# Kernel optimization log

Measured on AMD Instinct MI355X. Metric: run time of the kernel, lower is better.

The kernel has to match this reference:

```python
import jax, jax.numpy as jnp
import numpy as np

H = 4            # num_heads (forced: 128 projection / d_k=32)
DK = 32          # hardcoded d_k
SCALE = 1.0 / np.sqrt(32.0)
EPS = 1e-5       # LayerNorm eps (torch default)


def setup_inputs() -> dict:
    key = jax.random.key(0)
    ks = jax.random.split(key, 8)
    B, L, Dq, Dkv, M = 16, 4096, 512, 512, 512
    def w(k, shape, fan_in):
        return (jax.random.normal(k, shape, jnp.float32) / np.sqrt(fan_in)).astype(jnp.float32)
    return {
        "Q_in":  jax.random.normal(ks[0], (B, L, Dq),  jnp.float32),
        "KV_in": jax.random.normal(ks[1], (B, L, Dkv), jnp.float32),
        "Wq":  w(ks[2], (Dq, 128), Dq),   "bq":  jnp.zeros((128,), jnp.float32),
        "Wk":  w(ks[3], (Dkv, 128), Dkv), "bk":  jnp.zeros((128,), jnp.float32),
        "Wv":  w(ks[4], (Dkv, 128), Dkv), "bv":  jnp.zeros((128,), jnp.float32),
        "Wo":  w(ks[5], (128, M), 128),   "bo":  jnp.zeros((M,), jnp.float32),
        "Wqo": w(ks[6], (128, M), 128),   "bqo": jnp.zeros((M,), jnp.float32),
        "gamma": jnp.ones((M,), jnp.float32),
        "beta":  jnp.zeros((M,), jnp.float32),
    }


def reference(Q_in, KV_in, Wq, bq, Wk, bk, Wv, bv, Wo, bo, Wqo, bqo, gamma, beta):
    B, L, _ = Q_in.shape
    Qm = Q_in @ Wq + bq          # (B, L, 128)
    Km = KV_in @ Wk + bk         # (B, L, 128)
    Vm = KV_in @ Wv + bv         # (B, L, 128)

    def heads(X):
        # view(B, L, H, DK).permute(0, 2, 3, 1) -> (B, H, DK, L)
        return X.reshape(B, L, H, DK).transpose(0, 2, 3, 1)

    Qh, Kh, Vh = heads(Qm), heads(Km), heads(Vm)
    # matmul contracts over the SEQUENCE dim -> feature-feature scores (B,H,DK,DK)
    scores = jnp.einsum('bhdl,bhel->bhde', Qh, Kh) * SCALE
    attn = jax.nn.softmax(scores, axis=-1)          # dropout = identity (eval)
    out_h = jnp.einsum('bhde,bhel->bhdl', attn, Vh)  # (B, H, DK, L)
    out_h = out_h.transpose(0, 3, 1, 2).reshape(B, L, H * DK)  # (B, L, 128)

    out = out_h @ Wo + bo        # (B, L, M)
    Qm_ = Qm @ Wqo + bqo         # (B, L, M)
    x = Qm_ + out
    mu = jnp.mean(x, axis=-1, keepdims=True)
    var = jnp.var(x, axis=-1, keepdims=True)
    y = (x - mu) * jax.lax.rsqrt(var + EPS) * gamma + beta
    return (y, attn)
```

## Files before the change

### kernel.cpp

```cpp
#include <hip/hip_runtime.h>
#include <hip/hip_bf16.h>

typedef __bf16 bf16x8 __attribute__((ext_vector_type(8)));
typedef float  f32x4  __attribute__((ext_vector_type(4)));

#define SCALE_QK 0.17677669529663687f
#define LDSS 40

__device__ __forceinline__ float b2f(ushort u) {
    __hip_bfloat16 h; *reinterpret_cast<ushort*>(&h) = u; return __bfloat162float(h);
}
__device__ __forceinline__ ushort f2b(float f) {
    __hip_bfloat16 h = __float2bfloat16(f); return *reinterpret_cast<ushort*>(&h);
}

__global__ void k_prep(const float* __restrict__ Wq, const float* __restrict__ Wk,
                       const float* __restrict__ Wv, const float* __restrict__ Wqo,
                       const float* __restrict__ Wo,
                       ushort* __restrict__ WqThi, ushort* __restrict__ WqTlo,
                       ushort* __restrict__ WkThi, ushort* __restrict__ WkTlo,
                       ushort* __restrict__ WvT,  ushort* __restrict__ WqoT,
                       ushort* __restrict__ WoB) {
    int idx = blockIdx.x * 256 + threadIdx.x;
    int mat = idx >> 16, i = idx & 65535;
    if (mat == 0) {
        int n = i >> 9, k = i & 511;
        float w = Wq[k * 128 + n];
        ushort hi = f2b(w);
        WqThi[i] = hi; WqTlo[i] = f2b(w - b2f(hi));
    } else if (mat == 1) {
        int n = i >> 9, k = i & 511;
        float w = Wk[k * 128 + n];
        ushort hi = f2b(w);
        WkThi[i] = hi; WkTlo[i] = f2b(w - b2f(hi));
    } else if (mat == 2) {
        int n = i >> 9, k = i & 511;
        WvT[i] = f2b(Wv[k * 128 + n]);
    } else if (mat == 3) {
        int n = i >> 7, k = i & 127;
        WqoT[i] = f2b(Wqo[k * 512 + n]);
    } else if (mat == 4) {
        WoB[i] = f2b(Wo[i]);
    }
}

__global__ __launch_bounds__(256) void k_proj_split(
        const float* __restrict__ A, const ushort* __restrict__ BThi,
        const ushort* __restrict__ BTlo, const float* __restrict__ bias,
        float* __restrict__ outF, ushort* __restrict__ outB) {
    __shared__ __align__(16) ushort AsH[128 * LDSS], AsL[128 * LDSS];
    __shared__ __align__(16) ushort BsH[128 * LDSS], BsL[128 * LDSS];
    const int row0 = blockIdx.x * 128;
    const int tid  = threadIdx.x;
    const int wid  = tid >> 6, lane = tid & 63;
    const int wm = wid >> 1, wn = wid & 1;
    const int quad = lane >> 4, l16 = lane & 15;
    const int sr = tid >> 2;
    const int sc = (tid & 3) * 8;

    f32x4 acc[4][4] = {};

    for (int k0 = 0; k0 < 512; k0 += 32) {
        __syncthreads();
#pragma unroll
        for (int p = 0; p < 2; ++p) {
            int r = sr + p * 64;
            float4 a0 = *(const float4*)&A[(size_t)(row0 + r) * 512 + k0 + sc];
            float4 a1 = *(const float4*)&A[(size_t)(row0 + r) * 512 + k0 + sc + 4];
            float av[8] = {a0.x, a0.y, a0.z, a0.w, a1.x, a1.y, a1.z, a1.w};
            union { uint4 v; ushort u[8]; } H, L;
#pragma unroll
            for (int i = 0; i < 8; ++i) {
                ushort hi = f2b(av[i]);
                H.u[i] = hi;
                L.u[i] = f2b(av[i] - b2f(hi));
            }
            *(uint4*)&AsH[r * LDSS + sc] = H.v;
            *(uint4*)&AsL[r * LDSS + sc] = L.v;
            *(uint4*)&BsH[r * LDSS + sc] = *(const uint4*)&BThi[(size_t)r * 512 + k0 + sc];
            *(uint4*)&BsL[r * LDSS + sc] = *(const uint4*)&BTlo[(size_t)r * 512 + k0 + sc];
        }
        __syncthreads();
        bf16x8 aH[4], aL[4];
#pragma unroll
        for (int i = 0; i < 4; ++i) {
            int ro = (wm * 64 + i * 16 + l16) * LDSS + quad * 8;
            aH[i] = *reinterpret_cast<const bf16x8*>(&AsH[ro]);
            aL[i] = *reinterpret_cast<const bf16x8*>(&AsL[ro]);
        }
#pragma unroll
        for (int j = 0; j < 4; ++j) {
            int ro = (wn * 64 + j * 16 + l16) * LDSS + quad * 8;
            bf16x8 bH = *reinterpret_cast<const bf16x8*>(&BsH[ro]);
            bf16x8 bL = *reinterpret_cast<const bf16x8*>(&BsL[ro]);
#pragma unroll
            for (int i = 0; i < 4; ++i) {
                acc[i][j] = __builtin_amdgcn_mfma_f32_16x16x32_bf16(aL[i], bH, acc[i][j], 0, 0, 0);
                acc[i][j] = __builtin_amdgcn_mfma_f32_16x16x32_bf16(aH[i], bL, acc[i][j], 0, 0, 0);
                acc[i][j] = __builtin_amdgcn_mfma_f32_16x16x32_bf16(aH[i], bH, acc[i][j], 0, 0, 0);
            }
        }
    }

#pragma unroll
    for (int i = 0; i < 4; ++i)
#pragma unroll
        for (int j = 0; j < 4; ++j) {
            int ncol = wn * 64 + j * 16 + l16;
            float bv = bias[ncol];
#pragma unroll
            for (int r = 0; r < 4; ++r) {
                int mrow = row0 + wm * 64 + i * 16 + quad * 4 + r;
                float v = acc[i][j][r] + bv;
                if (outF) outF[(size_t)mrow * 128 + ncol] = v;
                if (outB) outB[(size_t)mrow * 128 + ncol] = f2b(v);
            }
        }
}

__global__ __launch_bounds__(256) void k_proj_kv(
        const float* __restrict__ A,
        const ushort* __restrict__ BKhi, const ushort* __restrict__ BKlo,
        const ushort* __restrict__ BV,
        const float* __restrict__ biasK, const float* __restrict__ biasV,
        float* __restrict__ KmF, ushort* __restrict__ VmB) {
    __shared__ __align__(16) ushort AsH[128 * LDSS], AsL[128 * LDSS];
    __shared__ __align__(16) ushort BsKH[128 * LDSS], BsKL[128 * LDSS], BsV[128 * LDSS];
    const int row0 = blockIdx.x * 128;
    const int tid  = threadIdx.x;
    const int wid  = tid >> 6, lane = tid & 63;
    const int wm = wid >> 1, wn = wid & 1;
    const int quad = lane >> 4, l16 = lane & 15;
    const int sr = tid >> 2;
    const int sc = (tid & 3) * 8;

    f32x4 accK[4][4] = {};
    f32x4 accV[4][4] = {};

    for (int k0 = 0; k0 < 512; k0 += 32) {
        __syncthreads();
#pragma unroll
        for (int p = 0; p < 2; ++p) {
            int r = sr + p * 64;
            float4 a0 = *(const float4*)&A[(size_t)(row0 + r) * 512 + k0 + sc];
            float4 a1 = *(const float4*)&A[(size_t)(row0 + r) * 512 + k0 + sc + 4];
            float av[8] = {a0.x, a0.y, a0.z, a0.w, a1.x, a1.y, a1.z, a1.w};
            union { uint4 v; ushort u[8]; } H, L;
#pragma unroll
            for (int i = 0; i < 8; ++i) {
                ushort hi = f2b(av[i]);
                H.u[i] = hi;
                L.u[i] = f2b(av[i] - b2f(hi));
            }
            *(uint4*)&AsH[r * LDSS + sc] = H.v;
            *(uint4*)&AsL[r * LDSS + sc] = L.v;
            *(uint4*)&BsKH[r * LDSS + sc] = *(const uint4*)&BKhi[(size_t)r * 512 + k0 + sc];
            *(uint4*)&BsKL[r * LDSS + sc] = *(const uint4*)&BKlo[(size_t)r * 512 + k0 + sc];
            *(uint4*)&BsV [r * LDSS + sc] = *(const uint4*)&BV  [(size_t)r * 512 + k0 + sc];
        }
        __syncthreads();
        bf16x8 aH[4], aL[4];
#pragma unroll
        for (int i = 0; i < 4; ++i) {
            int ro = (wm * 64 + i * 16 + l16) * LDSS + quad * 8;
            aH[i] = *reinterpret_cast<const bf16x8*>(&AsH[ro]);
            aL[i] = *reinterpret_cast<const bf16x8*>(&AsL[ro]);
        }
#pragma unroll
        for (int j = 0; j < 4; ++j) {
            int ro = (wn * 64 + j * 16 + l16) * LDSS + quad * 8;
            bf16x8 bKH = *reinterpret_cast<const bf16x8*>(&BsKH[ro]);
            bf16x8 bKL = *reinterpret_cast<const bf16x8*>(&BsKL[ro]);
            bf16x8 bV  = *reinterpret_cast<const bf16x8*>(&BsV [ro]);
#pragma unroll
            for (int i = 0; i < 4; ++i) {
                accK[i][j] = __builtin_amdgcn_mfma_f32_16x16x32_bf16(aL[i], bKH, accK[i][j], 0, 0, 0);
                accK[i][j] = __builtin_amdgcn_mfma_f32_16x16x32_bf16(aH[i], bKL, accK[i][j], 0, 0, 0);
                accK[i][j] = __builtin_amdgcn_mfma_f32_16x16x32_bf16(aH[i], bKH, accK[i][j], 0, 0, 0);
                accV[i][j] = __builtin_amdgcn_mfma_f32_16x16x32_bf16(aH[i], bV,  accV[i][j], 0, 0, 0);
            }
        }
    }

#pragma unroll
    for (int i = 0; i < 4; ++i)
#pragma unroll
        for (int j = 0; j < 4; ++j) {
            int ncol = wn * 64 + j * 16 + l16;
            float bk = biasK[ncol], bv = biasV[ncol];
#pragma unroll
            for (int r = 0; r < 4; ++r) {
                int mrow = row0 + wm * 64 + i * 16 + quad * 4 + r;
                KmF[(size_t)mrow * 128 + ncol] = accK[i][j][r] + bk;
                VmB[(size_t)mrow * 128 + ncol] = f2b(accV[i][j][r] + bv);
            }
        }
}

__global__ __launch_bounds__(256) void k_scores(
        const float* __restrict__ Qm, const float* __restrict__ Km,
        float* __restrict__ partial) {
    int b = blockIdx.x, sp = blockIdx.y;
    int t = threadIdx.x;
    int h = t >> 6, tl = t & 63;
    int d0 = (tl >> 3) * 4, e0 = (tl & 7) * 4;
    const float* Qb = Qm + ((size_t)b * 4096 + sp * 128) * 128 + h * 32 + d0;
    const float* Kb = Km + ((size_t)b * 4096 + sp * 128) * 128 + h * 32 + e0;
    float acc[4][4] = {};
#pragma unroll 4
    for (int l = 0; l < 128; ++l) {
        float4 q4 = *(const float4*)(Qb + (size_t)l * 128);
        float4 k4 = *(const float4*)(Kb + (size_t)l * 128);
        float q[4] = {q4.x, q4.y, q4.z, q4.w};
        float k[4] = {k4.x, k4.y, k4.z, k4.w};
#pragma unroll
        for (int i = 0; i < 4; ++i)
#pragma unroll
            for (int j = 0; j < 4; ++j) acc[i][j] += q[i] * k[j];
    }
    float* P = partial + ((size_t)(sp * 64 + b * 4 + h)) * 1024;
#pragma unroll
    for (int i = 0; i < 4; ++i)
#pragma unroll
        for (int j = 0; j < 4; ++j)
            P[(d0 + i) * 32 + e0 + j] = acc[i][j];
}

__global__ __launch_bounds__(256) void k_attn(
        const float* __restrict__ partial, const ushort* __restrict__ WoB,
        float* __restrict__ attnOut, ushort* __restrict__ WcT) {
    int bh = blockIdx.x; int b = bh >> 2, h = bh & 3;
    __shared__ float aS[1024];
    __shared__ __align__(16) ushort wS[32 * 512];
    int t = threadIdx.x;
    for (int i = t; i < 1024; i += 256) {
        float s = 0.f;
#pragma unroll
        for (int sp = 0; sp < 32; ++sp)
            s += partial[(size_t)(sp * 64 + bh) * 1024 + i];
        aS[i] = s * SCALE_QK;
    }
    for (int i = t; i < 2048; i += 256) {
        int r = i >> 6, c = (i & 63) * 8;
        *(uint4*)&wS[r * 512 + c] = *(const uint4*)&WoB[(size_t)(h * 32 + r) * 512 + c];
    }
    __syncthreads();
    if (t < 32) {
        float m = -1e30f;
#pragma unroll
        for (int e = 0; e < 32; ++e) m = fmaxf(m, aS[t * 32 + e]);
        float p[32]; float sum = 0.f;
#pragma unroll
        for (int e = 0; e < 32; ++e) { p[e] = __expf(aS[t * 32 + e] - m); sum += p[e]; }
        float inv = 1.f / sum;
#pragma unroll
        for (int e = 0; e < 32; ++e) aS[t * 32 + e] = p[e] * inv;
    }
    __syncthreads();
    for (int i = t; i < 1024; i += 256)
        attnOut[(size_t)bh * 1024 + i] = aS[i];
    int e = t & 31, mg = t >> 5;
    for (int mi = 0; mi < 64; ++mi) {
        int m = mg * 64 + mi;
        float acc = 0.f;
#pragma unroll
        for (int d = 0; d < 32; ++d)
            acc += aS[d * 32 + e] * b2f(wS[d * 512 + m]);
        WcT[((size_t)b * 512 + m) * 128 + h * 32 + e] = f2b(acc);
    }
}

__global__ __launch_bounds__(256) void k_out_ln(
        const ushort* __restrict__ Vm, const ushort* __restrict__ Qm,
        const ushort* __restrict__ WcT, const ushort* __restrict__ WqoT,
        const float* __restrict__ bo, const float* __restrict__ bqo,
        const float* __restrict__ gamma, const float* __restrict__ beta,
        float* __restrict__ Y) {
    __shared__ __align__(16) ushort As[64 * LDSS];
    __shared__ __align__(16) ushort Bs[512 * LDSS];
    __shared__ float sumS[4][64], sumSS[4][64], muA[64], rsA[64];
    const int row0 = blockIdx.x * 64;
    const int b = row0 >> 12;
    const ushort* WcTb = WcT + (size_t)b * 512 * 128;
    const int tid = threadIdx.x;
    const int wid = tid >> 6, lane = tid & 63;
    const int quad = lane >> 4, l16 = lane & 15;
    const int sr = tid >> 2;
    const int sc = (tid & 3) * 8;

    f32x4 acc[4][8] = {};

    for (int k0 = 0; k0 < 256; k0 += 32) {
        const ushort* Asrc; const ushort* Bsrc; int kk;
        if (k0 < 128) { Asrc = Vm; Bsrc = WcTb; kk = k0; }
        else          { Asrc = Qm; Bsrc = WqoT; kk = k0 - 128; }
        __syncthreads();
        *(uint4*)&As[sr * LDSS + sc] =
            *(const uint4*)&Asrc[(size_t)(row0 + sr) * 128 + kk + sc];
#pragma unroll
        for (int p = 0; p < 8; ++p) {
            int r = sr + p * 64;
            *(uint4*)&Bs[r * LDSS + sc] = *(const uint4*)&Bsrc[(size_t)r * 128 + kk + sc];
        }
        __syncthreads();
        bf16x8 aF[4];
#pragma unroll
        for (int i = 0; i < 4; ++i)
            aF[i] = *reinterpret_cast<const bf16x8*>(&As[(i * 16 + l16) * LDSS + quad * 8]);
#pragma unroll
        for (int j = 0; j < 8; ++j) {
            bf16x8 bF = *reinterpret_cast<const bf16x8*>(
                &Bs[(wid * 128 + j * 16 + l16) * LDSS + quad * 8]);
#pragma unroll
            for (int i = 0; i < 4; ++i)
                acc[i][j] = __builtin_amdgcn_mfma_f32_16x16x32_bf16(aF[i], bF, acc[i][j], 0, 0, 0);
        }
    }

    float bv[8];
#pragma unroll
    for (int j = 0; j < 8; ++j) {
        int ncol = wid * 128 + j * 16 + l16;
        bv[j] = bo[ncol] + bqo[ncol];
    }
    float sArr[4][4], ssArr[4][4];
#pragma unroll
    for (int i = 0; i < 4; ++i)
#pragma unroll
        for (int r = 0; r < 4; ++r) {
            float s = 0.f, ss = 0.f;
#pragma unroll
            for (int j = 0; j < 8; ++j) {
                float x = acc[i][j][r] + bv[j];
                s += x; ss += x * x;
            }
            sArr[i][r] = s; ssArr[i][r] = ss;
        }
#pragma unroll
    for (int off = 1; off < 16; off <<= 1)
#pragma unroll
        for (int i = 0; i < 4; ++i)
#pragma unroll
            for (int r = 0; r < 4; ++r) {
                sArr[i][r]  += __shfl_xor(sArr[i][r],  off, 64);
                ssArr[i][r] += __shfl_xor(ssArr[i][r], off, 64);
            }
    if (l16 == 0) {
#pragma unroll
        for (int i = 0; i < 4; ++i)
#pragma unroll
            for (int r = 0; r < 4; ++r) {
                int row = i * 16 + quad * 4 + r;
                sumS[wid][row]  = sArr[i][r];
                sumSS[wid][row] = ssArr[i][r];
            }
    }
    __syncthreads();
    if (tid < 64) {
        float s = sumS[0][tid] + sumS[1][tid] + sumS[2][tid] + sumS[3][tid];
        float ss = sumSS[0][tid] + sumSS[1][tid] + sumSS[2][tid] + sumSS[3][tid];
        float mu = s * (1.f / 512.f);
        float var = ss * (1.f / 512.f) - mu * mu;
        muA[tid] = mu;
        rsA[tid] = rsqrtf(var + 1e-5f);
    }
    __syncthreads();

    float gj[8], bj[8];
#pragma unroll
    for (int j = 0; j < 8; ++j) {
        int ncol = wid * 128 + j * 16 + l16;
        gj[j] = gamma[ncol]; bj[j] = beta[ncol];
    }
#pragma unroll
    for (int i = 0; i < 4; ++i)
#pragma unroll
        for (int r = 0; r < 4; ++r) {
            int row = i * 16 + quad * 4 + r;
            float mu = muA[row], rstd = rsA[row];
            size_t base = (size_t)(row0 + row) * 512 + wid * 128 + l16;
#pragma unroll
            for (int j = 0; j < 8; ++j) {
                float x = acc[i][j][r] + bv[j];
                Y[base + j * 16] = (x - mu) * rstd * gj[j] + bj[j];
            }
        }
}

extern "C" void kernel_launch(void* const* d_in, const int* in_sizes, int n_in,
                              void* d_out, int out_size, void* d_ws, size_t ws_size,
                              hipStream_t stream) {
    const float* Qin   = (const float*)d_in[0];
    const float* KVin  = (const float*)d_in[1];
    const float* Wq    = (const float*)d_in[2];
    const float* bq    = (const float*)d_in[3];
    const float* Wk    = (const float*)d_in[4];
    const float* bk    = (const float*)d_in[5];
    const float* Wv    = (const float*)d_in[6];
    const float* bv    = (const float*)d_in[7];
    const float* Wo    = (const float*)d_in[8];
    const float* bo    = (const float*)d_in[9];
    const float* Wqo   = (const float*)d_in[10];
    const float* bqo   = (const float*)d_in[11];
    const float* gamma = (const float*)d_in[12];
    const float* beta  = (const float*)d_in[13];
    float* out = (float*)d_out;
    float* attnOut = out + 33554432;

    char* ws = (char*)d_ws;
    ushort* WqThi = (ushort*)(ws);
    ushort* WqTlo = (ushort*)(ws + 131072);
    ushort* WkThi = (ushort*)(ws + 262144);
    ushort* WkTlo = (ushort*)(ws + 393216);
    ushort* WvT   = (ushort*)(ws + 524288);
    ushort* WqoT  = (ushort*)(ws + 655360);
    ushort* WoB   = (ushort*)(ws + 786432);
    float*  QmF   = (float*) (ws + 917504);
    float*  KmF   = (float*) (ws + 34471936);
    ushort* QmB   = (ushort*)(ws + 68026368);
    ushort* VmB   = (ushort*)(ws + 84803584);
    float*  part  = (float*) (ws + 101580800);
    ushort* WcT   = (ushort*)(ws + 109969408);

    k_prep<<<1280, 256, 0, stream>>>(Wq, Wk, Wv, Wqo, Wo,
                                     WqThi, WqTlo, WkThi, WkTlo, WvT, WqoT, WoB);
    k_proj_split<<<512, 256, 0, stream>>>(Qin, WqThi, WqTlo, bq, QmF, QmB);
    k_proj_kv<<<512, 256, 0, stream>>>(KVin, WkThi, WkTlo, WvT, bk, bv, KmF, VmB);
    k_scores<<<dim3(16, 32), 256, 0, stream>>>(QmF, KmF, part);
    k_attn<<<64, 256, 0, stream>>>(part, WoB, attnOut, WcT);
    k_out_ln<<<1024, 256, 0, stream>>>(VmB, QmB, WcT, WqoT, bo, bqo, gamma, beta, out);
}
```

Before: 485.9 us.

## Drop LDS staging in projection and output GEMMs; load fragments directly per wave

The projection and output/LayerNorm kernels no longer stage tiles in shared memory with block barriers. Each wave now owns 16 rows, loads its A fragment straight from global memory, and streams B (weight) fragments directly from global/L2. The LayerNorm reduction becomes wave-local, with no cross-wave shared-memory reduction. The scores kernel's sequence split is doubled (64 chunks of 64) for more blocks, and the workspace offset is moved to fit the larger partial buffer. This removes barriers and LDS traffic but gives up weight reuse across waves, so weight reads rise, and k_out_ln's 32 accumulators increase register pressure.

```diff
diff --git a/kernel.cpp b/kernel.cpp
--- a/kernel.cpp
+++ b/kernel.cpp
@@ -5,13 +5,27 @@
 typedef float  f32x4  __attribute__((ext_vector_type(4)));
 
 #define SCALE_QK 0.17677669529663687f
-#define LDSS 40
+#define MFMA(a, b, c) __builtin_amdgcn_mfma_f32_16x16x32_bf16((a), (b), (c), 0, 0, 0)
 
 __device__ __forceinline__ float b2f(ushort u) {
     __hip_bfloat16 h; *reinterpret_cast<ushort*>(&h) = u; return __bfloat162float(h);
 }
 __device__ __forceinline__ ushort f2b(float f) {
     __hip_bfloat16 h = __float2bfloat16(f); return *reinterpret_cast<ushort*>(&h);
+}
+__device__ __forceinline__ bf16x8 ld8(const ushort* p) {
+    union { uint4 v; bf16x8 f; } u; u.v = *(const uint4*)p; return u.f;
+}
+__device__ __forceinline__ void split8(float4 a0, float4 a1, bf16x8& hi, bf16x8& lo) {
+    float av[8] = {a0.x, a0.y, a0.z, a0.w, a1.x, a1.y, a1.z, a1.w};
+    union { bf16x8 f; ushort u[8]; } H, L;
+#pragma unroll
+    for (int i = 0; i < 8; ++i) {
+        ushort h = f2b(av[i]);
+        H.u[i] = h;
+        L.u[i] = f2b(av[i] - b2f(h));
+    }
+    hi = H.f; lo = L.f;
 }
 
 __global__ void k_prep(const float* __restrict__ Wq, const float* __restrict__ Wk,
@@ -44,78 +58,47 @@
     }
 }
 
-__global__ __launch_bounds__(256) void k_proj_split(
+__global__ __launch_bounds__(256) void k_proj_q(
         const float* __restrict__ A, const ushort* __restrict__ BThi,
         const ushort* __restrict__ BTlo, const float* __restrict__ bias,
         float* __restrict__ outF, ushort* __restrict__ outB) {
-    __shared__ __align__(16) ushort AsH[128 * LDSS], AsL[128 * LDSS];
-    __shared__ __align__(16) ushort BsH[128 * LDSS], BsL[128 * LDSS];
-    const int row0 = blockIdx.x * 128;
-    const int tid  = threadIdx.x;
-    const int wid  = tid >> 6, lane = tid & 63;
-    const int wm = wid >> 1, wn = wid & 1;
+    const int tid = threadIdx.x;
+    const int w = tid >> 6, lane = tid & 63;
     const int quad = lane >> 4, l16 = lane & 15;
-    const int sr = tid >> 2;
-    const int sc = (tid & 3) * 8;
-
-    f32x4 acc[4][4] = {};
+    const int wrow0 = blockIdx.x * 64 + w * 16;
+    const float* Ar = A + (size_t)(wrow0 + l16) * 512 + quad * 8;
+
+    f32x4 acc[8] = {};
 
     for (int k0 = 0; k0 < 512; k0 += 32) {
-        __syncthreads();
-#pragma unroll
-        for (int p = 0; p < 2; ++p) {
-            int r = sr + p * 64;
-            float4 a0 = *(const float4*)&A[(size_t)(row0 + r) * 512 + k0 + sc];
-            float4 a1 = *(const float4*)&A[(size_t)(row0 + r) * 512 + k0 + sc + 4];
-            float av[8] = {a0.x, a0.y, a0.z, a0.w, a1.x, a1.y, a1.z, a1.w};
-            union { uint4 v; ushort u[8]; } H, L;
-#pragma unroll
-            for (int i = 0; i < 8; ++i) {
-                ushort hi = f2b(av[i]);
-                H.u[i] = hi;
-                L.u[i] = f2b(av[i] - b2f(hi));
-            }
-            *(uint4*)&AsH[r * LDSS + sc] = H.v;
-            *(uint4*)&AsL[r * LDSS + sc] = L.v;
-            *(uint4*)&BsH[r * LDSS + sc] = *(const uint4*)&BThi[(size_t)r * 512 + k0 + sc];
-            *(uint4*)&BsL[r * LDSS + sc] = *(const uint4*)&BTlo[(size_t)r * 512 + k0 + sc];
-        }
-        __syncthreads();
-        bf16x8 aH[4], aL[4];
-#pragma unroll
-        for (int i = 0; i < 4; ++i) {
-            int ro = (wm * 64 + i * 16 + l16) * LDSS + quad * 8;
-            aH[i] = *reinterpret_cast<const bf16x8*>(&AsH[ro]);
-            aL[i] = *reinterpret_cast<const bf16x8*>(&AsL[ro]);
-        }
-#pragma unroll
-        for (int j = 0; j < 4; ++j) {
-            int ro = (wn * 64 + j * 16 + l16) * LDSS + quad * 8;
-            bf16x8 bH = *reinterpret_cast<const bf16x8*>(&BsH[ro]);
-            bf16x8 bL = *reinterpret_cast<const bf16x8*>(&BsL[ro]);
-#pragma unroll
-            for (int i = 0; i < 4; ++i) {
-                acc[i][j] = __builtin_amdgcn_mfma_f32_16x16x32_bf16(aL[i], bH, acc[i][j], 0, 0, 0);
-                acc[i][j] = __builtin_amdgcn_mfma_f32_16x16x32_bf16(aH[i], bL, acc[i][j], 0, 0, 0);
-                acc[i][j] = __builtin_amdgcn_mfma_f32_16x16x32_bf16(aH[i], bH, acc[i][j], 0, 0, 0);
-            }
-        }
-    }
-
-#pragma unroll
-    for (int i = 0; i < 4; ++i)
-#pragma unroll
-        for (int j = 0; j < 4; ++j) {
-            int ncol = wn * 64 + j * 16 + l16;
-            float bv = bias[ncol];
-#pragma unroll
-            for (int r = 0; r < 4; ++r) {
-                int mrow = row0 + wm * 64 + i * 16 + quad * 4 + r;
-                float v = acc[i][j][r] + bv;
-                if (outF) outF[(size_t)mrow * 128 + ncol] = v;
-                if (outB) outB[(size_t)mrow * 128 + ncol] = f2b(v);
-            }
-        }
+        float4 a0 = *(const float4*)(Ar + k0);
+        float4 a1 = *(const float4*)(Ar + k0 + 4);
+        bf16x8 aH, aL;
+        split8(a0, a1, aH, aL);
+        const int bofs = k0 + quad * 8;
+#pragma unroll
+        for (int j = 0; j < 8; ++j) {
+            const size_t bro = (size_t)(j * 16 + l16) * 512 + bofs;
+            bf16x8 bH = ld8(&BThi[bro]);
+            bf16x8 bL = ld8(&BTlo[bro]);
+            acc[j] = MFMA(aL, bH, acc[j]);
+            acc[j] = MFMA(aH, bL, acc[j]);
+            acc[j] = MFMA(aH, bH, acc[j]);
+        }
+    }
+
+    const int rbase = wrow0 + quad * 4;
+#pragma unroll
+    for (int j = 0; j < 8; ++j) {
+        int col = j * 16 + l16;
+        float bv = bias[col];
+#pragma unroll
+        for (int r = 0; r < 4; ++r) {
+            float v = acc[j][r] + bv;
+            outF[(size_t)(rbase + r) * 128 + col] = v;
+            outB[(size_t)(rbase + r) * 128 + col] = f2b(v);
+        }
+    }
 }
 
 __global__ __launch_bounds__(256) void k_proj_kv(
@@ -124,77 +107,45 @@
         const ushort* __restrict__ BV,
         const float* __restrict__ biasK, const float* __restrict__ biasV,
         float* __restrict__ KmF, ushort* __restrict__ VmB) {
-    __shared__ __align__(16) ushort AsH[128 * LDSS], AsL[128 * LDSS];
-    __shared__ __align__(16) ushort BsKH[128 * LDSS], BsKL[128 * LDSS], BsV[128 * LDSS];
-    const int row0 = blockIdx.x * 128;
-    const int tid  = threadIdx.x;
-    const int wid  = tid >> 6, lane = tid & 63;
-    const int wm = wid >> 1, wn = wid & 1;
+    const int tid = threadIdx.x;
+    const int w = tid >> 6, lane = tid & 63;
     const int quad = lane >> 4, l16 = lane & 15;
-    const int sr = tid >> 2;
-    const int sc = (tid & 3) * 8;
-
-    f32x4 accK[4][4] = {};
-    f32x4 accV[4][4] = {};
+    const int wrow0 = blockIdx.x * 64 + w * 16;
+    const float* Ar = A + (size_t)(wrow0 + l16) * 512 + quad * 8;
+
+    f32x4 accK[8] = {};
+    f32x4 accV[8] = {};
 
     for (int k0 = 0; k0 < 512; k0 += 32) {
-        __syncthreads();
-#pragma unroll
-        for (int p = 0; p < 2; ++p) {
-            int r = sr + p * 64;
-            float4 a0 = *(const float4*)&A[(size_t)(row0 + r) * 512 + k0 + sc];
-            float4 a1 = *(const float4*)&A[(size_t)(row0 + r) * 512 + k0 + sc + 4];
-            float av[8] = {a0.x, a0.y, a0.z, a0.w, a1.x, a1.y, a1.z, a1.w};
-            union { uint4 v; ushort u[8]; } H, L;
-#pragma unroll
-            for (int i = 0; i < 8; ++i) {
-                ushort hi = f2b(av[i]);
-                H.u[i] = hi;
-                L.u[i] = f2b(av[i] - b2f(hi));
-            }
-            *(uint4*)&AsH[r * LDSS + sc] = H.v;
-            *(uint4*)&AsL[r * LDSS + sc] = L.v;
-            *(uint4*)&BsKH[r * LDSS + sc] = *(const uint4*)&BKhi[(size_t)r * 512 + k0 + sc];
-            *(uint4*)&BsKL[r * LDSS + sc] = *(const uint4*)&BKlo[(size_t)r * 512 + k0 + sc];
-            *(uint4*)&BsV [r * LDSS + sc] = *(const uint4*)&BV  [(size_t)r * 512 + k0 + sc];
-        }
-        __syncthreads();
-        bf16x8 aH[4], aL[4];
-#pragma unroll
-        for (int i = 0; i < 4; ++i) {
-            int ro = (wm * 64 + i * 16 + l16) * LDSS + quad * 8;
-            aH[i] = *reinterpret_cast<const bf16x8*>(&AsH[ro]);
-            aL[i] = *reinterpret_cast<const bf16x8*>(&AsL[ro]);
-        }
-#pragma unroll
-        for (int j = 0; j < 4; ++j) {
-            int ro = (wn * 64 + j * 16 + l16) * LDSS + quad * 8;
-            bf16x8 bKH = *reinterpret_cast<const bf16x8*>(&BsKH[ro]);
-            bf16x8 bKL = *reinterpret_cast<const bf16x8*>(&BsKL[ro]);
-            bf16x8 bV  = *reinterpret_cast<const bf16x8*>(&BsV [ro]);
-#pragma unroll
-            for (int i = 0; i < 4; ++i) {
-                accK[i][j] = __builtin_amdgcn_mfma_f32_16x16x32_bf16(aL[i], bKH, accK[i][j], 0, 0, 0);
-                accK[i][j] = __builtin_amdgcn_mfma_f32_16x16x32_bf16(aH[i], bKL, accK[i][j], 0, 0, 0);
-                accK[i][j] = __builtin_amdgcn_mfma_f32_16x16x32_bf16(aH[i], bKH, accK[i][j], 0, 0, 0);
-                accV[i][j] = __builtin_amdgcn_mfma_f32_16x16x32_bf16(aH[i], bV,  accV[i][j], 0, 0, 0);
-            }
-        }
-    }
-
-#pragma unroll
-    for (int i = 0; i < 4; ++i)
-#pragma unroll
-        for (int j = 0; j < 4; ++j) {
-            int ncol = wn * 64 + j * 16 + l16;
-            float bk = biasK[ncol], bv = biasV[ncol];
-#pragma unroll
-            for (int r = 0; r < 4; ++r) {
-                int mrow = row0 + wm * 64 + i * 16 + quad * 4 + r;
-                KmF[(size_t)mrow * 128 + ncol] = accK[i][j][r] + bk;
-                VmB[(size_t)mrow * 128 + ncol] = f2b(accV[i][j][r] + bv);
-            }
-        }
+        float4 a0 = *(const float4*)(Ar + k0);
+        float4 a1 = *(const float4*)(Ar + k0 + 4);
+        bf16x8 aH, aL;
+        split8(a0, a1, aH, aL);
+        const int bofs = k0 + quad * 8;
+#pragma unroll
+        for (int j = 0; j < 8; ++j) {
+            const size_t bro = (size_t)(j * 16 + l16) * 512 + bofs;
+            bf16x8 bH = ld8(&BKhi[bro]);
+            bf16x8 bL = ld8(&BKlo[bro]);
+            bf16x8 bV = ld8(&BV[bro]);
+            accK[j] = MFMA(aL, bH, accK[j]);
+            accK[j] = MFMA(aH, bL, accK[j]);
+            accK[j] = MFMA(aH, bH, accK[j]);
+            accV[j] = MFMA(aH, bV, accV[j]);
+        }
+    }
+
+    const int rbase = wrow0 + quad * 4;
+#pragma unroll
+    for (int j = 0; j < 8; ++j) {
+        int col = j * 16 + l16;
+        float bk = biasK[col], bv = biasV[col];
+#pragma unroll
+        for (int r = 0; r < 4; ++r) {
+            KmF[(size_t)(rbase + r) * 128 + col] = accK[j][r] + bk;
+            VmB[(size_t)(rbase + r) * 128 + col] = f2b(accV[j][r] + bv);
+        }
+    }
 }
 
 __global__ __launch_bounds__(256) void k_scores(
@@ -204,11 +155,11 @@
     int t = threadIdx.x;
     int h = t >> 6, tl = t & 63;
     int d0 = (tl >> 3) * 4, e0 = (tl & 7) * 4;
-    const float* Qb = Qm + ((size_t)b * 4096 + sp * 128) * 128 + h * 32 + d0;
-    const float* Kb = Km + ((size_t)b * 4096 + sp * 128) * 128 + h * 32 + e0;
+    const float* Qb = Qm + ((size_t)b * 4096 + sp * 64) * 128 + h * 32 + d0;
+    const float* Kb = Km + ((size_t)b * 4096 + sp * 64) * 128 + h * 32 + e0;
     float acc[4][4] = {};
-#pragma unroll 4
-    for (int l = 0; l < 128; ++l) {
+#pragma unroll 8
+    for (int l = 0; l < 64; ++l) {
         float4 q4 = *(const float4*)(Qb + (size_t)l * 128);
         float4 k4 = *(const float4*)(Kb + (size_t)l * 128);
         float q[4] = {q4.x, q4.y, q4.z, q4.w};
@@ -236,7 +187,7 @@
     for (int i = t; i < 1024; i += 256) {
         float s = 0.f;
 #pragma unroll
-        for (int sp = 0; sp < 32; ++sp)
+        for (int sp = 0; sp < 64; ++sp)
             s += partial[(size_t)(sp * 64 + bh) * 1024 + i];
         aS[i] = s * SCALE_QK;
     }
@@ -276,115 +227,64 @@
         const float* __restrict__ bo, const float* __restrict__ bqo,
         const float* __restrict__ gamma, const float* __restrict__ beta,
         float* __restrict__ Y) {
-    __shared__ __align__(16) ushort As[64 * LDSS];
-    __shared__ __align__(16) ushort Bs[512 * LDSS];
-    __shared__ float sumS[4][64], sumSS[4][64], muA[64], rsA[64];
-    const int row0 = blockIdx.x * 64;
-    const int b = row0 >> 12;
+    const int tid = threadIdx.x;
+    const int w = tid >> 6, lane = tid & 63;
+    const int quad = lane >> 4, l16 = lane & 15;
+    const int wrow0 = blockIdx.x * 64 + w * 16;
+    const int b = wrow0 >> 12;
     const ushort* WcTb = WcT + (size_t)b * 512 * 128;
-    const int tid = threadIdx.x;
-    const int wid = tid >> 6, lane = tid & 63;
-    const int quad = lane >> 4, l16 = lane & 15;
-    const int sr = tid >> 2;
-    const int sc = (tid & 3) * 8;
-
-    f32x4 acc[4][8] = {};
-
+
+    f32x4 acc[32] = {};
+
+#pragma unroll
     for (int k0 = 0; k0 < 256; k0 += 32) {
-        const ushort* Asrc; const ushort* Bsrc; int kk;
-        if (k0 < 128) { Asrc = Vm; Bsrc = WcTb; kk = k0; }
-        else          { Asrc = Qm; Bsrc = WqoT; kk = k0 - 128; }
-        __syncthreads();
-        *(uint4*)&As[sr * LDSS + sc] =
-            *(const uint4*)&Asrc[(size_t)(row0 + sr) * 128 + kk + sc];
-#pragma unroll
-        for (int p = 0; p < 8; ++p) {
-            int r = sr + p * 64;
-            *(uint4*)&Bs[r * LDSS + sc] = *(const uint4*)&Bsrc[(size_t)r * 128 + kk + sc];
-        }
-        __syncthreads();
-        bf16x8 aF[4];
-#pragma unroll
-        for (int i = 0; i < 4; ++i)
-            aF[i] = *reinterpret_cast<const bf16x8*>(&As[(i * 16 + l16) * LDSS + quad * 8]);
-#pragma unroll
-        for (int j = 0; j < 8; ++j) {
-            bf16x8 bF = *reinterpret_cast<const bf16x8*>(
-                &Bs[(wid * 128 + j * 16 + l16) * LDSS + quad * 8]);
-#pragma unroll
-            for (int i = 0; i < 4; ++i)
-                acc[i][j] = __builtin_amdgcn_mfma_f32_16x16x32_bf16(aF[i], bF, acc[i][j], 0, 0, 0);
-        }
-    }
-
-    float bv[8];
-#pragma unroll
-    for (int j = 0; j < 8; ++j) {
-        int ncol = wid * 128 + j * 16 + l16;
-        bv[j] = bo[ncol] + bqo[ncol];
-    }
-    float sArr[4][4], ssArr[4][4];
-#pragma unroll
-    for (int i = 0; i < 4; ++i)
+        const ushort* Asrc = (k0 < 128) ? Vm : Qm;
+        const ushort* Bsrc = (k0 < 128) ? WcTb : WqoT;
+        const int kk = (k0 < 128) ? k0 : (k0 - 128);
+        bf16x8 aF = ld8(&Asrc[(size_t)(wrow0 + l16) * 128 + kk + quad * 8]);
+        const int bofs = kk + quad * 8;
+#pragma unroll
+        for (int j = 0; j < 32; ++j) {
+            bf16x8 bF = ld8(&Bsrc[(size_t)(j * 16 + l16) * 128 + bofs]);
+            acc[j] = MFMA(aF, bF, acc[j]);
+        }
+    }
+
+    float s[4] = {0.f, 0.f, 0.f, 0.f}, ss[4] = {0.f, 0.f, 0.f, 0.f};
+#pragma unroll
+    for (int j = 0; j < 32; ++j) {
+        int col = j * 16 + l16;
+        float bv = bo[col] + bqo[col];
 #pragma unroll
         for (int r = 0; r < 4; ++r) {
-            float s = 0.f, ss = 0.f;
-#pragma unroll
-            for (int j = 0; j < 8; ++j) {
-                float x = acc[i][j][r] + bv[j];
-                s += x; ss += x * x;
-            }
-            sArr[i][r] = s; ssArr[i][r] = ss;
-        }
+            float x = acc[j][r] + bv;
+            acc[j][r] = x;
+            s[r] += x; ss[r] += x * x;
+        }
+    }
 #pragma unroll
     for (int off = 1; off < 16; off <<= 1)
 #pragma unroll
-        for (int i = 0; i < 4; ++i)
-#pragma unroll
-            for (int r = 0; r < 4; ++r) {
-                sArr[i][r]  += __shfl_xor(sArr[i][r],  off, 64);
-                ssArr[i][r] += __shfl_xor(ssArr[i][r], off, 64);
-            }
-    if (l16 == 0) {
-#pragma unroll
-        for (int i = 0; i < 4; ++i)
-#pragma unroll
-            for (int r = 0; r < 4; ++r) {
-                int row = i * 16 + quad * 4 + r;
-                sumS[wid][row]  = sArr[i][r];
-                sumSS[wid][row] = ssArr[i][r];
-            }
-    }
-    __syncthreads();
-    if (tid < 64) {
-        float s = sumS[0][tid] + sumS[1][tid] + sumS[2][tid] + sumS[3][tid];
-        float ss = sumSS[0][tid] + sumSS[1][tid] + sumSS[2][tid] + sumSS[3][tid];
-        float mu = s * (1.f / 512.f);
-        float var = ss * (1.f / 512.f) - mu * mu;
-        muA[tid] = mu;
-        rsA[tid] = rsqrtf(var + 1e-5f);
-    }
-    __syncthreads();
-
-    float gj[8], bj[8];
-#pragma unroll
-    for (int j = 0; j < 8; ++j) {
-        int ncol = wid * 128 + j * 16 + l16;
-        gj[j] = gamma[ncol]; bj[j] = beta[ncol];
-    }
-#pragma unroll
-    for (int i = 0; i < 4; ++i)
-#pragma unroll
         for (int r = 0; r < 4; ++r) {
-            int row = i * 16 + quad * 4 + r;
-            float mu = muA[row], rstd = rsA[row];
-            size_t base = (size_t)(row0 + row) * 512 + wid * 128 + l16;
-#pragma unroll
-            for (int j = 0; j < 8; ++j) {
-                float x = acc[i][j][r] + bv[j];
-                Y[base + j * 16] = (x - mu) * rstd * gj[j] + bj[j];
-            }
-        }
+            s[r]  += __shfl_xor(s[r],  off, 64);
+            ss[r] += __shfl_xor(ss[r], off, 64);
+        }
+    float mu[4], rs[4];
+#pragma unroll
+    for (int r = 0; r < 4; ++r) {
+        mu[r] = s[r] * (1.f / 512.f);
+        float var = ss[r] * (1.f / 512.f) - mu[r] * mu[r];
+        rs[r] = rsqrtf(var + 1e-5f);
+    }
+    const int rbase = wrow0 + quad * 4;
+#pragma unroll
+    for (int j = 0; j < 32; ++j) {
+        int col = j * 16 + l16;
+        float g = gamma[col], be = beta[col];
+#pragma unroll
+        for (int r = 0; r < 4; ++r)
+            Y[(size_t)(rbase + r) * 512 + col] = (acc[j][r] - mu[r]) * rs[r] * g + be;
+    }
 }
 
 extern "C" void kernel_launch(void* const* d_in, const int* in_sizes, int n_in,
@@ -420,13 +320,13 @@
     ushort* QmB   = (ushort*)(ws + 68026368);
     ushort* VmB   = (ushort*)(ws + 84803584);
     float*  part  = (float*) (ws + 101580800);
-    ushort* WcT   = (ushort*)(ws + 109969408);
+    ushort* WcT   = (ushort*)(ws + 118358016);
 
     k_prep<<<1280, 256, 0, stream>>>(Wq, Wk, Wv, Wqo, Wo,
                                      WqThi, WqTlo, WkThi, WkTlo, WvT, WqoT, WoB);
-    k_proj_split<<<512, 256, 0, stream>>>(Qin, WqThi, WqTlo, bq, QmF, QmB);
-    k_proj_kv<<<512, 256, 0, stream>>>(KVin, WkThi, WkTlo, WvT, bk, bv, KmF, VmB);
-    k_scores<<<dim3(16, 32), 256, 0, stream>>>(QmF, KmF, part);
+    k_proj_q<<<1024, 256, 0, stream>>>(Qin, WqThi, WqTlo, bq, QmF, QmB);
+    k_proj_kv<<<1024, 256, 0, stream>>>(KVin, WkThi, WkTlo, WvT, bk, bv, KmF, VmB);
+    k_scores<<<dim3(16, 64), 256, 0, stream>>>(QmF, KmF, part);
     k_attn<<<64, 256, 0, stream>>>(part, WoB, attnOut, WcT);
     k_out_ln<<<1024, 256, 0, stream>>>(VmB, QmB, WcT, WqoT, bo, bqo, gamma, beta, out);
 }
```

New measurement: 817.8 us. +68.3%, slower.
